# Optimization experiments

Measured on AMD Instinct MI355X. Metric: run time of the kernel, lower is better.

The kernel has to match this reference:

```python
import jax, jax.numpy as jnp
import numpy as np

FEATURE_DIM = 256
HEADS = 8


def setup_inputs() -> dict:
    key = jax.random.key(0)
    ks = jax.random.split(key, 9)
    d, h = FEATURE_DIM, HEADS
    b, n = 4, 4096
    s_in = 1.0 / np.sqrt(d)
    s_out = 1.0 / np.sqrt(d * h)
    return {
        "x": jax.random.normal(ks[0], (b, n, d), dtype=jnp.float32),
        "Wq": jax.random.uniform(ks[1], (d, d * h), jnp.float32, -s_in, s_in),
        "bq": jax.random.uniform(ks[2], (d * h,), jnp.float32, -s_in, s_in),
        "Wk": jax.random.uniform(ks[3], (d, d * h), jnp.float32, -s_in, s_in),
        "bk": jax.random.uniform(ks[4], (d * h,), jnp.float32, -s_in, s_in),
        "Wv": jax.random.uniform(ks[5], (d, d * h), jnp.float32, -s_in, s_in),
        "bv": jax.random.uniform(ks[6], (d * h,), jnp.float32, -s_in, s_in),
        "Wo": jax.random.uniform(ks[7], (d * h, d), jnp.float32, -s_out, s_out),
        "bo": jax.random.uniform(ks[8], (d,), jnp.float32, -s_out, s_out),
    }


def reference(x, Wq, bq, Wk, bk, Wv, bv, Wo, bo):
    b, n, d = x.shape
    h = HEADS
    scale = d ** (-0.5)
    # projections: (b, n, h, d) -- note: NO head transpose, matching original
    q = (x @ Wq + bq).reshape(b, n, h, d)
    k = (x @ Wk + bk).reshape(b, n, h, d)
    v = (x @ Wv + bv).reshape(b, n, h, d)
    # attention is head-vs-head per token: (b, n, h, h)
    attn = jnp.einsum("bnhd,bngd->bnhg", q, k) * scale
    attn = jax.nn.softmax(attn, axis=-1)
    out = jnp.einsum("bnhg,bngd->bnhd", attn, v).reshape(b, n, h * d)
    return out @ Wo + bo
```

## Files before the change

kernel.cpp:

```cpp
#include <hip/hip_runtime.h>
#include <hip/hip_bf16.h>
#include <math.h>

typedef __bf16 bf16;
typedef __bf16 bf16x4 __attribute__((ext_vector_type(4)));
typedef __bf16 bf16x8 __attribute__((ext_vector_type(8)));
typedef float f32x4 __attribute__((ext_vector_type(4)));
typedef unsigned int u32;
typedef u32 __attribute__((address_space(1))) gu32;
typedef u32 __attribute__((address_space(3))) lu32;

#define TOK   16384
#define D_    256
#define HD    2048
#define QKVN  6144

#define GLDS16(g, l) __builtin_amdgcn_global_load_lds((gu32*)(g), (lu32*)(l), 16, 0, 0)
#define WAIT_VM(n) __builtin_amdgcn_s_waitcnt(0x0F70 | (n))

__device__ __forceinline__ void transpose_body(
    const void* __restrict__ src, bf16* __restrict__ dst, int R, int C,
    int tc, int tr, int f, int mode, float (*tile)[33])
{
    int lx = threadIdx.x & 31, ly = threadIdx.x >> 5;
    for (int i = 0; i < 4; i++) {
        int r = ly + i * 8;
        size_t idx = (size_t)(tr + r) * C + tc + lx;
        tile[r][lx] = f ? ((const float*)src)[idx] : (float)((const bf16*)src)[idx];
    }
    __syncthreads();
    for (int i = 0; i < 4; i++) {
        int r = ly + i * 8;
        int k = tr + lx;
        int n = tc + r;
        size_t di;
        if (mode == 1)      di = (size_t)n * R + (size_t)(k & 255) * 8 + (k >> 8);
        else if (mode == 2) di = (size_t)(((n & 255) << 3) | (n >> 8)) * R + k;
        else                di = (size_t)n * R + k;
        dst[di] = (bf16)tile[lx][r];
    }
}

__global__ __launch_bounds__(256) void prep(
    const void* __restrict__ x,
    const void* __restrict__ Wq, const void* __restrict__ bq,
    const void* __restrict__ Wk, const void* __restrict__ bk,
    const void* __restrict__ Wv, const void* __restrict__ bv,
    const void* __restrict__ Wo, const void* __restrict__ bo,
    bf16* __restrict__ xb, bf16* __restrict__ WT, bf16* __restrict__ WoT,
    bf16* __restrict__ bqkv, bf16* __restrict__ bob)
{
    __shared__ float tile[32][33];
    __shared__ int sflag;
    int tid = threadIdx.x;
    if (tid == 0) sflag = 0;
    __syncthreads();
    {
        float v = fabsf((float)((const bf16*)x)[2 * tid]);
        if (!(v < 1e4f)) sflag = 1;
    }
    __syncthreads();
    int f = sflag;
    int b = blockIdx.x;

    if (b < 4096) {
        int i = b * 256 + tid;
        bf16x4 o;
        if (f) { f32x4 v = ((const f32x4*)x)[i]; for (int e = 0; e < 4; e++) o[e] = (bf16)v[e]; }
        else   { o = ((const bf16x4*)x)[i]; }
        ((bf16x4*)xb)[i] = o;
    } else if (b < 4121) {
        int i = (b - 4096) * 256 + tid;
        if (i < 6400) {
            const void* src; bf16* dst; int off, woff;
            if (i < 2048)      { src = bq; dst = bqkv;        off = i;        woff = off; }
            else if (i < 4096) { src = bk; dst = bqkv + 2048; off = i - 2048; woff = off; }
            else if (i < 6144) { src = bv; dst = bqkv + 4096; off = i - 4096;
                                 woff = ((off & 255) << 3) | (off >> 8); }
            else               { src = bo; dst = bob;         off = i - 6144; woff = off; }
            float v = f ? ((const float*)src)[off] : (float)((const bf16*)src)[off];
            dst[woff] = (bf16)v;
        }
        __syncthreads();
    } else if (b < 5657) {
        int idx = b - 4121;
        int tx = idx & 63, rest = idx >> 6;
        int ty = rest & 7, tz = rest >> 3;
        const void* src = (tz == 0) ? Wq : (tz == 1) ? Wk : Wv;
        bf16* dst = WT + (size_t)tz * 2048 * 256;
        transpose_body(src, dst, 256, 2048, tx * 32, ty * 32, f, (tz == 2) ? 2 : 0, tile);
    } else {
        int idx = b - 5657;
        int tx = idx & 7, ty = idx >> 3;
        transpose_body(Wo, WoT, 2048, 256, tx * 32, ty * 32, f, 1, tile);
    }
}

__global__ __launch_bounds__(256) void proj_gemm(
    const bf16* __restrict__ X, const bf16* __restrict__ WT,
    const bf16* __restrict__ bqkv, bf16* __restrict__ qkv)
{
    __shared__ char smem[36864];
    bf16* As = (bf16*)smem;
    bf16* Bs = (bf16*)(smem + 16384);
    int m0 = blockIdx.y * 128, n0 = blockIdx.x * 128;
    int tid = threadIdx.x, wave = tid >> 6, lane = tid & 63;
    int wm = (wave >> 1) * 64, wn = (wave & 1) * 64;
    int mrow = lane & 15, quad = lane >> 4;
    int lrow8 = lane >> 3, lslot = lane & 7;

    f32x4 acc[4][4] = {};
    for (int k0 = 0; k0 < D_; k0 += 64) {
        __syncthreads();
        for (int i = 0; i < 4; i++) {
            int rbase = wave * 32 + i * 8;
            int row = rbase + lrow8;
            int gc = lslot ^ (row & 7);
            GLDS16(&X[(size_t)(m0 + row) * D_ + k0 + gc * 8], &As[rbase * 64]);
            GLDS16(&WT[(size_t)(n0 + row) * D_ + k0 + gc * 8], &Bs[rbase * 64]);
        }
        __syncthreads();
        for (int kk = 0; kk < 64; kk += 32) {
            int slot = (((kk >> 3) + quad) ^ (mrow & 7)) * 8;
            bf16x8 af[4], bfv[4];
            for (int mt = 0; mt < 4; mt++)
                af[mt] = *(const bf16x8*)&As[(wm + mt * 16 + mrow) * 64 + slot];
            for (int nt = 0; nt < 4; nt++)
                bfv[nt] = *(const bf16x8*)&Bs[(wn + nt * 16 + mrow) * 64 + slot];
            for (int mt = 0; mt < 4; mt++)
                for (int nt = 0; nt < 4; nt++)
                    acc[mt][nt] = __builtin_amdgcn_mfma_f32_16x16x32_bf16(
                        bfv[nt], af[mt], acc[mt][nt], 0, 0, 0);
        }
    }

    __syncthreads();
    bf16* ep = (bf16*)smem + wave * (64 * 72);
    for (int mt = 0; mt < 4; mt++) {
        for (int nt = 0; nt < 4; nt++) {
            int col = n0 + wn + nt * 16 + quad * 4;
            bf16x4 bb = *(const bf16x4*)&bqkv[col];
            bf16x4 o;
            for (int r = 0; r < 4; r++) o[r] = (bf16)(acc[mt][nt][r] + (float)bb[r]);
            *(bf16x4*)&ep[(mt * 16 + mrow) * 72 + nt * 16 + quad * 4] = o;
        }
    }
    __syncthreads();
    for (int i = 0; i < 8; i++) {
        int r = i * 8 + (lane >> 3);
        int cb = (lane & 7) * 8;
        bf16x8 val = *(const bf16x8*)&ep[r * 72 + cb];
        *(bf16x8*)&qkv[(size_t)(m0 + wm + r) * QKVN + n0 + wn + cb] = val;
    }
}

__device__ __forceinline__ void stage_qk(const bf16* __restrict__ qkv,
                                         bf16* dstb, int t, int lane)
{
    const bf16* base = qkv + (size_t)t * QKVN;
#pragma unroll
    for (int i = 0; i < 8; i++) {
        int s = i * 64 + lane;
        int row = s >> 5, cs = s & 31;
        int gc = cs ^ (row & 7);
        GLDS16(base + row * 256 + gc * 8, (char*)dstb + i * 1024);
    }
}

__global__ __launch_bounds__(256) void attn_score(
    const bf16* __restrict__ qkv, float* __restrict__ P)
{
    __shared__ bf16 sh[4][2][4096];
    int wave = threadIdx.x >> 6, lane = threadIdx.x & 63;
    int h = lane >> 3, g = lane & 7;
    int wid = blockIdx.x * 4 + wave;
    int t0 = wid * 8;

    stage_qk(qkv, sh[wave][0], t0, lane);
    for (int ti = 0; ti < 8; ti++) {
        if (ti < 7) {
            stage_qk(qkv, sh[wave][(ti + 1) & 1], t0 + ti + 1, lane);
            WAIT_VM(8);
        } else {
            WAIT_VM(0);
        }
        const bf16* buf = sh[wave][ti & 1];
        const bf16* qrow = buf + h * 256;
        const bf16* krow = buf + (8 + g) * 256;
        float s0 = 0.f, s1 = 0.f, s2 = 0.f, s3 = 0.f;
        for (int c = 0; c < 32; c += 4) {
            bf16x8 a0 = *(const bf16x8*)&qrow[((c + 0) ^ h) * 8];
            bf16x8 b0 = *(const bf16x8*)&krow[((c + 0) ^ g) * 8];
            bf16x8 a1 = *(const bf16x8*)&qrow[((c + 1) ^ h) * 8];
            bf16x8 b1 = *(const bf16x8*)&krow[((c + 1) ^ g) * 8];
            bf16x8 a2 = *(const bf16x8*)&qrow[((c + 2) ^ h) * 8];
            bf16x8 b2 = *(const bf16x8*)&krow[((c + 2) ^ g) * 8];
            bf16x8 a3 = *(const bf16x8*)&qrow[((c + 3) ^ h) * 8];
            bf16x8 b3 = *(const bf16x8*)&krow[((c + 3) ^ g) * 8];
            for (int e = 0; e < 8; e++) {
                s0 += (float)a0[e] * (float)b0[e];
                s1 += (float)a1[e] * (float)b1[e];
                s2 += (float)a2[e] * (float)b2[e];
                s3 += (float)a3[e] * (float)b3[e];
            }
        }
        float s = ((s0 + s1) + (s2 + s3)) * 0.0625f;
        float m = s;
        for (int off = 1; off < 8; off <<= 1) m = fmaxf(m, __shfl_xor(m, off, 8));
        float p = __expf(s - m);
        float sum = p;
        for (int off = 1; off < 8; off <<= 1) sum += __shfl_xor(sum, off, 8);
        P[(size_t)(t0 + ti) * 64 + lane] = p / sum;
    }
}

__global__ __launch_bounds__(256) void out_fused(
    const bf16* __restrict__ qkv, const bf16* __restrict__ WoT,
    const float* __restrict__ P, const bf16* __restrict__ bob,
    float* __restrict__ outp)
{
    __shared__ bf16 Bs[2][256 * 64];
    __shared__ bf16 Vs[2][32 * 64];
    int m0 = blockIdx.x * 32;
    int tid = threadIdx.x, wave = tid >> 6, lane = tid & 63;
    int wm = (wave >> 1) * 16, wn = (wave & 1) * 128;
    int mrow = lane & 15, quad = lane >> 4;
    int t = wm + mrow, ts = t & 7;
    int sl8 = lane >> 3, sl = lane & 7;

    float Pv[64];
    {
        const float* pr = P + (size_t)(m0 + t) * 64;
#pragma unroll
        for (int j = 0; j < 16; j++) {
            f32x4 v4 = *(const f32x4*)&pr[j * 4];
            Pv[4 * j + 0] = v4[0]; Pv[4 * j + 1] = v4[1];
            Pv[4 * j + 2] = v4[2]; Pv[4 * j + 3] = v4[3];
        }
    }

#define STAGE(bb, cc) {                                                        \
        int tt = (wave << 3) + sl8;                                            \
        GLDS16(&qkv[(size_t)(m0 + tt) * QKVN + 4096 + (cc) * 64                \
                    + ((sl ^ (tt & 7)) << 3)], &Vs[bb][wave * 512]);           \
        for (int i = 0; i < 8; i++) {                                          \
            int n = (wave << 6) + (i << 3) + sl8;                              \
            GLDS16(&WoT[(size_t)n * HD + (cc) * 64 + ((sl ^ (n & 7)) << 3)],   \
                   &Bs[bb][(wave << 6) + (i << 3) << 6]);                      \
        } }

    f32x4 acc[8] = {};
    {
        int tt = (wave << 3) + sl8;
        GLDS16(&qkv[(size_t)(m0 + tt) * QKVN + 4096 + ((sl ^ (tt & 7)) << 3)],
               &Vs[0][wave * 512]);
#pragma unroll
        for (int i = 0; i < 8; i++) {
            int n = (wave << 6) + (i << 3) + sl8;
            GLDS16(&WoT[(size_t)n * HD + ((sl ^ (n & 7)) << 3)],
                   &Bs[0][((wave << 6) + (i << 3)) << 6]);
        }
    }

    for (int c = 0; c < 32; c++) {
        __syncthreads();
        if (c < 31) {
            int cc = c + 1, bb = cc & 1;
            int tt = (wave << 3) + sl8;
            GLDS16(&qkv[(size_t)(m0 + tt) * QKVN + 4096 + cc * 64
                        + ((sl ^ (tt & 7)) << 3)], &Vs[bb][wave * 512]);
#pragma unroll
            for (int i = 0; i < 8; i++) {
                int n = (wave << 6) + (i << 3) + sl8;
                GLDS16(&WoT[(size_t)n * HD + cc * 64 + ((sl ^ (n & 7)) << 3)],
                       &Bs[bb][((wave << 6) + (i << 3)) << 6]);
            }
        }
        const bf16* Vb = Vs[c & 1];
        const bf16* Bb = Bs[c & 1];

        bf16x8 vf0 = *(const bf16x8*)&Vb[(t << 6) + ((quad ^ ts) << 3)];
        bf16x8 vf1 = *(const bf16x8*)&Vb[(t << 6) + (((quad + 4) ^ ts) << 3)];
        float v0f[8], v1f[8];
#pragma unroll
        for (int e = 0; e < 8; e++) { v0f[e] = (float)vf0[e]; v1f[e] = (float)vf1[e]; }
        bf16x8 af0, af1;
#pragma unroll
        for (int hh = 0; hh < 8; hh++) {
            float a0 = 0.f, a1 = 0.f;
#pragma unroll
            for (int gg = 0; gg < 8; gg++) {
                a0 += Pv[hh * 8 + gg] * v0f[gg];
                a1 += Pv[hh * 8 + gg] * v1f[gg];
            }
            af0[hh] = (bf16)a0; af1[hh] = (bf16)a1;
        }
#pragma unroll
        for (int nt = 0; nt < 8; nt++) {
            bf16x8 bv = *(const bf16x8*)&Bb[(wn + nt * 16 + mrow) * 64
                            + ((quad ^ (mrow & 7)) << 3)];
            acc[nt] = __builtin_amdgcn_mfma_f32_16x16x32_bf16(bv, af0, acc[nt], 0, 0, 0);
        }
#pragma unroll
        for (int nt = 0; nt < 8; nt++) {
            bf16x8 bv = *(const bf16x8*)&Bb[(wn + nt * 16 + mrow) * 64
                            + (((4 + quad) ^ (mrow & 7)) << 3)];
            acc[nt] = __builtin_amdgcn_mfma_f32_16x16x32_bf16(bv, af1, acc[nt], 0, 0, 0);
        }
    }
#undef STAGE

    int row = m0 + wm + mrow;
#pragma unroll
    for (int nt = 0; nt < 8; nt++) {
        int col = wn + nt * 16 + quad * 4;
        bf16x4 bb = *(const bf16x4*)&bob[col];
        f32x4 o;
        for (int r = 0; r < 4; r++) o[r] = acc[nt][r] + (float)bb[r];
        *(f32x4*)&outp[(size_t)row * D_ + col] = o;
    }
}

extern "C" void kernel_launch(void* const* d_in, const int* in_sizes, int n_in,
                              void* d_out, int out_size, void* d_ws, size_t ws_size,
                              hipStream_t stream)
{
    const void* x  = d_in[0];
    const void* Wq = d_in[1];
    const void* bq = d_in[2];
    const void* Wk = d_in[3];
    const void* bk = d_in[4];
    const void* Wv = d_in[5];
    const void* bv = d_in[6];
    const void* Wo = d_in[7];
    const void* bo = d_in[8];
    float* out = (float*)d_out;

    char* ws = (char*)d_ws;
    bf16* qkv  = (bf16*)ws;
    bf16* WT   = (bf16*)(ws + 201326592);
    bf16* WoT  = (bf16*)(ws + 204472320);
    bf16* xb   = (bf16*)(ws + 205520896);
    bf16* bqkv = (bf16*)(ws + 213909504);
    bf16* bob  = (bf16*)(ws + 213921792);
    float* Pbuf = (float*)xb;

    prep<<<6169, 256, 0, stream>>>(x, Wq, bq, Wk, bk, Wv, bv, Wo, bo,
                                   xb, WT, WoT, bqkv, bob);
    proj_gemm<<<dim3(48, 128), 256, 0, stream>>>(xb, WT, bqkv, qkv);
    attn_score<<<512, 256, 0, stream>>>(qkv, Pbuf);
    out_fused<<<512, 256, 0, stream>>>(qkv, WoT, Pbuf, bob, out);
}
```

Before: 235.0 us.

## Fuse QKV projection with head-vs-head score computation, avoid Q/K global writes

Replaces the separate projection GEMM and score kernel with one kernel where each block keeps 64 tokens of X in registers and streams interleaved Q/K/V weight tiles. Q and K tiles are reduced into per-token head scores in LDS immediately, and only V is written to global memory. Weight and bias layouts are permuted in prep so Q and K columns for matching dims arrive together. This removes the Q/K round trip through HBM and a launch, but the grid is only 256 blocks with many barriers per step, which may limit occupancy and parallelism.

```diff
diff --git a/kernel.cpp b/kernel.cpp
--- a/kernel.cpp
+++ b/kernel.cpp
@@ -13,10 +13,12 @@
 #define TOK   16384
 #define D_    256
 #define HD    2048
-#define QKVN  6144
+#define VN    2048
 
 #define GLDS16(g, l) __builtin_amdgcn_global_load_lds((gu32*)(g), (lu32*)(l), 16, 0, 0)
-#define WAIT_VM(n) __builtin_amdgcn_s_waitcnt(0x0F70 | (n))
+#define WAIT_VM(n)  __builtin_amdgcn_s_waitcnt(0x0F70 | (n))
+#define WAIT_LGKM0  __builtin_amdgcn_s_waitcnt(0xC07F)
+#define BAR() do { __builtin_amdgcn_s_barrier(); __builtin_amdgcn_sched_barrier(0); } while (0)
 
 __device__ __forceinline__ void transpose_body(
     const void* __restrict__ src, bf16* __restrict__ dst, int R, int C,
@@ -34,9 +36,16 @@
         int k = tr + lx;
         int n = tc + r;
         size_t di;
-        if (mode == 1)      di = (size_t)n * R + (size_t)(k & 255) * 8 + (k >> 8);
-        else if (mode == 2) di = (size_t)(((n & 255) << 3) | (n >> 8)) * R + k;
-        else                di = (size_t)n * R + k;
+        if (mode == 1)
+            di = (size_t)n * 2048 + ((k & 255) << 3) + (k >> 8);
+        else if (mode == 2)
+            di = (size_t)(4096 + ((n & 255) << 3) + (n >> 8)) * 256 + k;
+        else if (mode == 3)
+            di = (size_t)((((n & 255) >> 4) << 8) + ((n >> 8) << 4) + (n & 15)) * 256 + k;
+        else if (mode == 4)
+            di = (size_t)((((n & 255) >> 4) << 8) + 128 + ((n >> 8) << 4) + (n & 15)) * 256 + k;
+        else
+            di = (size_t)n * R + k;
         dst[di] = (bf16)tile[lx][r];
     }
 }
@@ -47,7 +56,7 @@
     const void* __restrict__ Wk, const void* __restrict__ bk,
     const void* __restrict__ Wv, const void* __restrict__ bv,
     const void* __restrict__ Wo, const void* __restrict__ bo,
-    bf16* __restrict__ xb, bf16* __restrict__ WT, bf16* __restrict__ WoT,
+    bf16* __restrict__ xb, bf16* __restrict__ WTI, bf16* __restrict__ WoT,
     bf16* __restrict__ bqkv, bf16* __restrict__ bob)
 {
     __shared__ float tile[32][33];
@@ -72,12 +81,21 @@
     } else if (b < 4121) {
         int i = (b - 4096) * 256 + tid;
         if (i < 6400) {
-            const void* src; bf16* dst; int off, woff;
-            if (i < 2048)      { src = bq; dst = bqkv;        off = i;        woff = off; }
-            else if (i < 4096) { src = bk; dst = bqkv + 2048; off = i - 2048; woff = off; }
-            else if (i < 6144) { src = bv; dst = bqkv + 4096; off = i - 4096;
-                                 woff = ((off & 255) << 3) | (off >> 8); }
-            else               { src = bo; dst = bob;         off = i - 6144; woff = off; }
+            const void* src; bf16* dst = bqkv; int off, woff;
+            if (i < 2048) {
+                src = bq; off = i;
+                int d = off & 255, h = off >> 8;
+                woff = ((d >> 4) << 8) + (h << 4) + (d & 15);
+            } else if (i < 4096) {
+                src = bk; off = i - 2048;
+                int d = off & 255, h = off >> 8;
+                woff = ((d >> 4) << 8) + 128 + (h << 4) + (d & 15);
+            } else if (i < 6144) {
+                src = bv; off = i - 4096;
+                woff = 4096 + ((off & 255) << 3) + (off >> 8);
+            } else {
+                src = bo; dst = bob; off = i - 6144; woff = off;
+            }
             float v = f ? ((const float*)src)[off] : (float)((const bf16*)src)[off];
             dst[woff] = (bf16)v;
         }
@@ -87,8 +105,8 @@
         int tx = idx & 63, rest = idx >> 6;
         int ty = rest & 7, tz = rest >> 3;
         const void* src = (tz == 0) ? Wq : (tz == 1) ? Wk : Wv;
-        bf16* dst = WT + (size_t)tz * 2048 * 256;
-        transpose_body(src, dst, 256, 2048, tx * 32, ty * 32, f, (tz == 2) ? 2 : 0, tile);
+        int mode = (tz == 0) ? 3 : (tz == 1) ? 4 : 2;
+        transpose_body(src, WTI, 256, 2048, tx * 32, ty * 32, f, mode, tile);
     } else {
         int idx = b - 5657;
         int tx = idx & 7, ty = idx >> 3;
@@ -96,126 +114,151 @@
     }
 }
 
-__global__ __launch_bounds__(256) void proj_gemm(
-    const bf16* __restrict__ X, const bf16* __restrict__ WT,
-    const bf16* __restrict__ bqkv, bf16* __restrict__ qkv)
-{
-    __shared__ char smem[36864];
-    bf16* As = (bf16*)smem;
-    bf16* Bs = (bf16*)(smem + 16384);
-    int m0 = blockIdx.y * 128, n0 = blockIdx.x * 128;
+__global__ __launch_bounds__(512, 2) void qkv_score(
+    const bf16* __restrict__ X, const bf16* __restrict__ WTI,
+    const bf16* __restrict__ bI, bf16* __restrict__ vout, float* __restrict__ P)
+{
+    __shared__ bf16 Ws[2][64 * 256];
+    __shared__ bf16 qkh[64 * 256];
     int tid = threadIdx.x, wave = tid >> 6, lane = tid & 63;
-    int wm = (wave >> 1) * 64, wn = (wave & 1) * 64;
     int mrow = lane & 15, quad = lane >> 4;
-    int lrow8 = lane >> 3, lslot = lane & 7;
-
-    f32x4 acc[4][4] = {};
-    for (int k0 = 0; k0 < D_; k0 += 64) {
-        __syncthreads();
-        for (int i = 0; i < 4; i++) {
-            int rbase = wave * 32 + i * 8;
-            int row = rbase + lrow8;
-            int gc = lslot ^ (row & 7);
-            GLDS16(&X[(size_t)(m0 + row) * D_ + k0 + gc * 8], &As[rbase * 64]);
-            GLDS16(&WT[(size_t)(n0 + row) * D_ + k0 + gc * 8], &Bs[rbase * 64]);
-        }
-        __syncthreads();
-        for (int kk = 0; kk < 64; kk += 32) {
-            int slot = (((kk >> 3) + quad) ^ (mrow & 7)) * 8;
-            bf16x8 af[4], bfv[4];
-            for (int mt = 0; mt < 4; mt++)
-                af[mt] = *(const bf16x8*)&As[(wm + mt * 16 + mrow) * 64 + slot];
-            for (int nt = 0; nt < 4; nt++)
-                bfv[nt] = *(const bf16x8*)&Bs[(wn + nt * 16 + mrow) * 64 + slot];
-            for (int mt = 0; mt < 4; mt++)
-                for (int nt = 0; nt < 4; nt++)
-                    acc[mt][nt] = __builtin_amdgcn_mfma_f32_16x16x32_bf16(
-                        bfv[nt], af[mt], acc[mt][nt], 0, 0, 0);
-        }
-    }
-
-    __syncthreads();
-    bf16* ep = (bf16*)smem + wave * (64 * 72);
-    for (int mt = 0; mt < 4; mt++) {
-        for (int nt = 0; nt < 4; nt++) {
-            int col = n0 + wn + nt * 16 + quad * 4;
-            bf16x4 bb = *(const bf16x4*)&bqkv[col];
-            bf16x4 o;
-            for (int r = 0; r < 4; r++) o[r] = (bf16)(acc[mt][nt][r] + (float)bb[r]);
-            *(bf16x4*)&ep[(mt * 16 + mrow) * 72 + nt * 16 + quad * 4] = o;
-        }
-    }
-    __syncthreads();
-    for (int i = 0; i < 8; i++) {
-        int r = i * 8 + (lane >> 3);
-        int cb = (lane & 7) * 8;
-        bf16x8 val = *(const bf16x8*)&ep[r * 72 + cb];
-        *(bf16x8*)&qkv[(size_t)(m0 + wm + r) * QKVN + n0 + wn + cb] = val;
-    }
-}
-
-__device__ __forceinline__ void stage_qk(const bf16* __restrict__ qkv,
-                                         bf16* dstb, int t, int lane)
-{
-    const bf16* base = qkv + (size_t)t * QKVN;
-#pragma unroll
-    for (int i = 0; i < 8; i++) {
-        int s = i * 64 + lane;
-        int row = s >> 5, cs = s & 31;
-        int gc = cs ^ (row & 7);
-        GLDS16(base + row * 256 + gc * 8, (char*)dstb + i * 1024);
-    }
-}
-
-__global__ __launch_bounds__(256) void attn_score(
-    const bf16* __restrict__ qkv, float* __restrict__ P)
-{
-    __shared__ bf16 sh[4][2][4096];
-    int wave = threadIdx.x >> 6, lane = threadIdx.x & 63;
+    int wm3 = (wave >> 2) * 32, wn3 = (wave & 3) * 16;
     int h = lane >> 3, g = lane & 7;
-    int wid = blockIdx.x * 4 + wave;
-    int t0 = wid * 8;
-
-    stage_qk(qkv, sh[wave][0], t0, lane);
-    for (int ti = 0; ti < 8; ti++) {
-        if (ti < 7) {
-            stage_qk(qkv, sh[wave][(ti + 1) & 1], t0 + ti + 1, lane);
-            WAIT_VM(8);
+    int t0 = blockIdx.x * 64;
+
+#pragma unroll
+    for (int i = 0; i < 4; i++) {
+        int row = (i * 8 + wave) * 2 + (lane >> 5);
+        int sl = lane & 31;
+        int gc = (sl & 24) | ((sl & 7) ^ (row & 7));
+        GLDS16(&X[(size_t)(t0 + row) * 256 + gc * 8], &Ws[0][(i * 8 + wave) * 512]);
+    }
+    WAIT_VM(0);
+    BAR();
+    bf16x8 areg[2][8];
+#pragma unroll
+    for (int mt = 0; mt < 2; mt++)
+#pragma unroll
+        for (int ks = 0; ks < 8; ks++) {
+            int arow = wm3 + mt * 16 + mrow;
+            int sl = ks * 4 + quad;
+            int ph = (sl & 24) | ((sl & 7) ^ (arow & 7));
+            areg[mt][ks] = *(const bf16x8*)&Ws[0][arow * 256 + ph * 8];
+        }
+    WAIT_LGKM0;
+    BAR();
+
+#pragma unroll
+    for (int i = 0; i < 4; i++) {
+        int row = (i * 8 + wave) * 2 + (lane >> 5);
+        int sl = lane & 31;
+        int gc = (sl & 24) | ((sl & 7) ^ (row & 7));
+        GLDS16(&WTI[(size_t)row * 256 + gc * 8], &Ws[0][(i * 8 + wave) * 512]);
+    }
+
+    float S[8] = {};
+
+    for (int s = 0; s < 96; s++) {
+        int cur = s & 1;
+        if (s < 95) {
+#pragma unroll
+            for (int i = 0; i < 4; i++) {
+                int row = (i * 8 + wave) * 2 + (lane >> 5);
+                int sl = lane & 31;
+                int gc = (sl & 24) | ((sl & 7) ^ (row & 7));
+                GLDS16(&WTI[(size_t)((s + 1) * 64 + row) * 256 + gc * 8],
+                       &Ws[cur ^ 1][(i * 8 + wave) * 512]);
+            }
+            WAIT_VM(4);
         } else {
             WAIT_VM(0);
         }
-        const bf16* buf = sh[wave][ti & 1];
-        const bf16* qrow = buf + h * 256;
-        const bf16* krow = buf + (8 + g) * 256;
-        float s0 = 0.f, s1 = 0.f, s2 = 0.f, s3 = 0.f;
-        for (int c = 0; c < 32; c += 4) {
-            bf16x8 a0 = *(const bf16x8*)&qrow[((c + 0) ^ h) * 8];
-            bf16x8 b0 = *(const bf16x8*)&krow[((c + 0) ^ g) * 8];
-            bf16x8 a1 = *(const bf16x8*)&qrow[((c + 1) ^ h) * 8];
-            bf16x8 b1 = *(const bf16x8*)&krow[((c + 1) ^ g) * 8];
-            bf16x8 a2 = *(const bf16x8*)&qrow[((c + 2) ^ h) * 8];
-            bf16x8 b2 = *(const bf16x8*)&krow[((c + 2) ^ g) * 8];
-            bf16x8 a3 = *(const bf16x8*)&qrow[((c + 3) ^ h) * 8];
-            bf16x8 b3 = *(const bf16x8*)&krow[((c + 3) ^ g) * 8];
-            for (int e = 0; e < 8; e++) {
-                s0 += (float)a0[e] * (float)b0[e];
-                s1 += (float)a1[e] * (float)b1[e];
-                s2 += (float)a2[e] * (float)b2[e];
-                s3 += (float)a3[e] * (float)b3[e];
-            }
-        }
-        float s = ((s0 + s1) + (s2 + s3)) * 0.0625f;
-        float m = s;
+        BAR();
+
+        f32x4 acc0 = {}, acc1 = {};
+        int brow = wn3 + mrow;
+#pragma unroll
+        for (int ks = 0; ks < 8; ks++) {
+            int sl = ks * 4 + quad;
+            int ph = (sl & 24) | ((sl & 7) ^ (brow & 7));
+            bf16x8 bv = *(const bf16x8*)&Ws[cur][brow * 256 + ph * 8];
+            acc0 = __builtin_amdgcn_mfma_f32_16x16x32_bf16(bv, areg[0][ks], acc0, 0, 0, 0);
+            acc1 = __builtin_amdgcn_mfma_f32_16x16x32_bf16(bv, areg[1][ks], acc1, 0, 0, 0);
+        }
+
+        if (s < 64) {
+            int sub = s & 3, qk = sub >> 1;
+            int hh = (sub & 1) * 4 + (wn3 >> 4);
+            bf16x4 bb = *(const bf16x4*)&bI[s * 64 + wn3 + quad * 4];
+#pragma unroll
+            for (int mt = 0; mt < 2; mt++) {
+                int t = wm3 + mt * 16 + mrow;
+                f32x4 a = mt ? acc1 : acc0;
+                bf16x4 o;
+#pragma unroll
+                for (int r = 0; r < 4; r++) o[r] = (bf16)(a[r] + (float)bb[r]);
+                int bo = ((qk << 8) + (hh << 5) + (quad << 3)) ^ ((t & 7) << 4);
+                *(bf16x4*)((char*)qkh + t * 512 + bo) = o;
+            }
+            WAIT_LGKM0;
+            BAR();
+            if ((s & 3) == 3) {
+#pragma unroll
+                for (int ti = 0; ti < 8; ti++) {
+                    int t = wave * 8 + ti;
+                    int swz = (t & 7) << 4;
+                    const char* base = (const char*)qkh + t * 512;
+                    bf16x8 q0 = *(const bf16x8*)(base + (((h << 5)) ^ swz));
+                    bf16x8 q1 = *(const bf16x8*)(base + (((h << 5) + 16) ^ swz));
+                    bf16x8 k0 = *(const bf16x8*)(base + ((256 + (g << 5)) ^ swz));
+                    bf16x8 k1 = *(const bf16x8*)(base + ((256 + (g << 5) + 16) ^ swz));
+                    float a = 0.f;
+#pragma unroll
+                    for (int e = 0; e < 8; e++)
+                        a += (float)q0[e] * (float)k0[e] + (float)q1[e] * (float)k1[e];
+                    S[ti] += a;
+                }
+                WAIT_LGKM0;
+            }
+        } else {
+            int sv = s - 64;
+            bf16* ep = qkh;
+            bf16x4 bb = *(const bf16x4*)&bI[s * 64 + wn3 + quad * 4];
+#pragma unroll
+            for (int mt = 0; mt < 2; mt++) {
+                int t = wm3 + mt * 16 + mrow;
+                f32x4 a = mt ? acc1 : acc0;
+                bf16x4 o;
+#pragma unroll
+                for (int r = 0; r < 4; r++) o[r] = (bf16)(a[r] + (float)bb[r]);
+                *(bf16x4*)&ep[t * 72 + wn3 + quad * 4] = o;
+            }
+            WAIT_LGKM0;
+            BAR();
+            {
+                int tt = tid >> 3, c8 = (tid & 7) * 8;
+                bf16x8 val = *(const bf16x8*)&ep[tt * 72 + c8];
+                *(bf16x8*)&vout[(size_t)(t0 + tt) * VN + sv * 64 + c8] = val;
+            }
+            BAR();
+        }
+    }
+
+#pragma unroll
+    for (int ti = 0; ti < 8; ti++) {
+        int t = t0 + wave * 8 + ti;
+        float sc = S[ti] * 0.0625f;
+        float m = sc;
         for (int off = 1; off < 8; off <<= 1) m = fmaxf(m, __shfl_xor(m, off, 8));
-        float p = __expf(s - m);
+        float p = __expf(sc - m);
         float sum = p;
         for (int off = 1; off < 8; off <<= 1) sum += __shfl_xor(sum, off, 8);
-        P[(size_t)(t0 + ti) * 64 + lane] = p / sum;
+        P[(size_t)t * 64 + lane] = p / sum;
     }
 }
 
 __global__ __launch_bounds__(256) void out_fused(
-    const bf16* __restrict__ qkv, const bf16* __restrict__ WoT,
+    const bf16* __restrict__ vb, const bf16* __restrict__ WoT,
     const float* __restrict__ P, const bf16* __restrict__ bob,
     float* __restrict__ outp)
 {
@@ -239,20 +282,10 @@
         }
     }
 
-#define STAGE(bb, cc) {                                                        \
-        int tt = (wave << 3) + sl8;                                            \
-        GLDS16(&qkv[(size_t)(m0 + tt) * QKVN + 4096 + (cc) * 64                \
-                    + ((sl ^ (tt & 7)) << 3)], &Vs[bb][wave * 512]);           \
-        for (int i = 0; i < 8; i++) {                                          \
-            int n = (wave << 6) + (i << 3) + sl8;                              \
-            GLDS16(&WoT[(size_t)n * HD + (cc) * 64 + ((sl ^ (n & 7)) << 3)],   \
-                   &Bs[bb][(wave << 6) + (i << 3) << 6]);                      \
-        } }
-
     f32x4 acc[8] = {};
     {
         int tt = (wave << 3) + sl8;
-        GLDS16(&qkv[(size_t)(m0 + tt) * QKVN + 4096 + ((sl ^ (tt & 7)) << 3)],
+        GLDS16(&vb[(size_t)(m0 + tt) * VN + ((sl ^ (tt & 7)) << 3)],
                &Vs[0][wave * 512]);
 #pragma unroll
         for (int i = 0; i < 8; i++) {
@@ -267,8 +300,8 @@
         if (c < 31) {
             int cc = c + 1, bb = cc & 1;
             int tt = (wave << 3) + sl8;
-            GLDS16(&qkv[(size_t)(m0 + tt) * QKVN + 4096 + cc * 64
-                        + ((sl ^ (tt & 7)) << 3)], &Vs[bb][wave * 512]);
+            GLDS16(&vb[(size_t)(m0 + tt) * VN + cc * 64 + ((sl ^ (tt & 7)) << 3)],
+                   &Vs[bb][wave * 512]);
 #pragma unroll
             for (int i = 0; i < 8; i++) {
                 int n = (wave << 6) + (i << 3) + sl8;
@@ -308,7 +341,6 @@
             acc[nt] = __builtin_amdgcn_mfma_f32_16x16x32_bf16(bv, af1, acc[nt], 0, 0, 0);
         }
     }
-#undef STAGE
 
     int row = m0 + wm + mrow;
 #pragma unroll
@@ -337,17 +369,16 @@
     float* out = (float*)d_out;
 
     char* ws = (char*)d_ws;
-    bf16* qkv  = (bf16*)ws;
-    bf16* WT   = (bf16*)(ws + 201326592);
-    bf16* WoT  = (bf16*)(ws + 204472320);
-    bf16* xb   = (bf16*)(ws + 205520896);
-    bf16* bqkv = (bf16*)(ws + 213909504);
-    bf16* bob  = (bf16*)(ws + 213921792);
-    float* Pbuf = (float*)xb;
+    bf16*  vbuf = (bf16*)ws;
+    bf16*  WTI  = (bf16*)(ws + 67108864);
+    bf16*  WoT  = (bf16*)(ws + 70254592);
+    bf16*  xb   = (bf16*)(ws + 71303168);
+    bf16*  bqkv = (bf16*)(ws + 79691776);
+    bf16*  bob  = (bf16*)(ws + 79704064);
+    float* Pbuf = (float*)(ws + 79704576);
 
     prep<<<6169, 256, 0, stream>>>(x, Wq, bq, Wk, bk, Wv, bv, Wo, bo,
-                                   xb, WT, WoT, bqkv, bob);
-    proj_gemm<<<dim3(48, 128), 256, 0, stream>>>(xb, WT, bqkv, qkv);
-    attn_score<<<512, 256, 0, stream>>>(qkv, Pbuf);
-    out_fused<<<512, 256, 0, stream>>>(qkv, WoT, Pbuf, bob, out);
-}
+                                   xb, WTI, WoT, bqkv, bob);
+    qkv_score<<<256, 512, 0, stream>>>(xb, WTI, bqkv, vbuf, Pbuf);
+    out_fused<<<512, 256, 0, stream>>>(vbuf, WoT, Pbuf, bob, out);
+}
```

New measurement: 271.8 us. 15.7% more time.
